# Performance work log

Measured on AMD Instinct MI355X. Metric: run time of the kernel, lower is better.

The kernel has to match this reference:

```python
import jax, jax.numpy as jnp
import numpy as np


def _deform_conv2d(x, offset, weight, stride=(1, 1), pad=(1, 1), dilation=(1, 1)):
    # x: [B,C,H,W]; offset: [B, 2*Goff*kh*kw, oh, ow]; weight: [OC, C//Gw, kh, kw]
    B, C, H, W = x.shape
    OC, Cg, kh, kw = weight.shape
    Gw = C // Cg
    K = kh * kw
    sh, sw = stride
    ph, pw = pad
    dh, dw = dilation
    oh = (H + 2 * ph - (dh * (kh - 1) + 1)) // sh + 1
    ow = (W + 2 * pw - (dw * (kw - 1) + 1)) // sw + 1
    Goff = offset.shape[1] // (2 * K)
    # torchvision layout: per offset group, per kernel tap k, (dy, dx)
    off = offset.reshape(B, Goff, K, 2, oh, ow)
    ki = jnp.arange(K) // kw  # kernel row per tap
    kj = jnp.arange(K) % kw   # kernel col per tap
    base_y = jnp.arange(oh) * sh - ph
    base_x = jnp.arange(ow) * sw - pw
    gy = (base_y[None, :] + (ki * dh)[:, None]).astype(x.dtype)  # [K, oh]
    gx = (base_x[None, :] + (kj * dw)[:, None]).astype(x.dtype)  # [K, ow]
    py = off[:, :, :, 0] + gy[None, None, :, :, None]  # [B,Goff,K,oh,ow]
    px = off[:, :, :, 1] + gx[None, None, :, None, :]
    cpg = C // Goff  # channels per offset group
    py = jnp.repeat(py, cpg, axis=1)  # [B,C,K,oh,ow]
    px = jnp.repeat(px, cpg, axis=1)
    xf = x.reshape(B, C, H * W)
    y0 = jnp.floor(py)
    x0 = jnp.floor(px)
    ty = py - y0
    tx = px - x0
    y0i = y0.astype(jnp.int32)
    x0i = x0.astype(jnp.int32)

    def gather(cy, cx):
        valid = (cy >= 0) & (cy < H) & (cx >= 0) & (cx < W)
        idx = jnp.clip(cy, 0, H - 1) * W + jnp.clip(cx, 0, W - 1)
        v = jnp.take_along_axis(xf, idx.reshape(B, C, -1), axis=2).reshape(idx.shape)
        return jnp.where(valid, v, jnp.zeros((), x.dtype))

    # bilinear sample, zero padding outside image (matches torchvision)
    v = (gather(y0i, x0i) * (1 - ty) * (1 - tx)
         + gather(y0i, x0i + 1) * (1 - ty) * tx
         + gather(y0i + 1, x0i) * ty * (1 - tx)
         + gather(y0i + 1, x0i + 1) * ty * tx)  # [B,C,K,oh,ow]
    v = v.reshape(B, Gw, Cg, K, oh, ow)
    wg = weight.reshape(Gw, OC // Gw, Cg, K)
    out = jnp.einsum('bgckhw,gock->bgohw', v, wg)
    return out.reshape(B, OC, oh, ow)


def setup_inputs() -> dict:
    key = jax.random.key(0)
    k1, k2, k3 = jax.random.split(key, 3)
    x = jax.random.normal(k1, (8, 64, 56, 56), dtype=jnp.float32)
    offset = jax.random.normal(k2, (8, 18, 56, 56), dtype=jnp.float32)
    weight = jax.random.normal(k3, (64, 64, 3, 3), dtype=jnp.float32) * 0.05
    return {"input": x, "offset": offset, "weight": weight}


def reference(input, offset, weight):
    return _deform_conv2d(input, offset, weight, stride=(1, 1), pad=(1, 1), dilation=(1, 1))
```

## Files before the change

### kernel.cpp

```cpp
#include <hip/hip_runtime.h>
#include <hip/hip_fp16.h>


typedef _Float16 f16x8 __attribute__((ext_vector_type(8)));
typedef float    f32x4 __attribute__((ext_vector_type(4)));

namespace {
constexpr int Bn = 8, Cn = 64, Hn = 56, Wn = 56;
constexpr int Kk = 9, OCn = 64;
constexpr int NPIX = 56 * 56;
constexpr int CK   = Cn * Kk;
constexpr int TP   = 32;
constexpr int TILES = NPIX / TP;
constexpr int XTILES = NPIX / 64;
constexpr int KSTEPS = CK / 32;
}

__device__ __forceinline__ __half2 u2h(unsigned u) {
    union { unsigned u; __half2 h; } x; x.u = u; return x.h;
}
__device__ __forceinline__ unsigned bcast_h(float f) {
    unsigned short hs = __half_as_ushort(__float2half(f));
    return (unsigned)hs * 0x10001u;
}
__device__ __forceinline__ void lds_barrier() {
    asm volatile("s_waitcnt lgkmcnt(0)" ::: "memory");
    __builtin_amdgcn_s_barrier();
}

__global__ __launch_bounds__(256) void prep_kernel(
    const float* __restrict__ x, const float* __restrict__ w,
    unsigned short* __restrict__ xh, unsigned short* __restrict__ wh2)
{
    const int tid = threadIdx.x;
    if (blockIdx.x >= 392) {
        const int i = (blockIdx.x - 392) * 256 + tid;
        if (i < OCn * CK) {
            const int j    = i & 7;
            const int lane = (i >> 3) & 63;
            const int rest = i >> 9;
            const int og   = rest / KSTEPS;
            const int oc   = og * 16 + (lane & 15);
            const int kglob = (rest % KSTEPS) * 32 + (lane >> 4) * 8 + j;
            const int tap = kglob >> 6;
            const int c   = kglob & 63;
            wh2[i] = __half_as_ushort(__float2half(w[oc * CK + c * Kk + tap]));
        }
        return;
    }
    __shared__ unsigned short lds[64][66];
    const int b  = blockIdx.x / XTILES;
    const int t0 = (blockIdx.x % XTILES) * 64;
    const float* xb = x + (size_t)b * Cn * NPIX;
    {
        const int hw0 = (tid & 15) * 4;
        #pragma unroll
        for (int i = 0; i < 4; ++i) {
            const int c = (tid >> 4) + i * 16;
            const float4 v = *(const float4*)(xb + (size_t)c * NPIX + t0 + hw0);
            lds[hw0 + 0][c] = __half_as_ushort(__float2half(v.x));
            lds[hw0 + 1][c] = __half_as_ushort(__float2half(v.y));
            lds[hw0 + 2][c] = __half_as_ushort(__float2half(v.z));
            lds[hw0 + 3][c] = __half_as_ushort(__float2half(v.w));
        }
    }
    __syncthreads();
    {
        const int co = (tid & 7) * 8;
        #pragma unroll
        for (int i = 0; i < 2; ++i) {
            const int hw = (tid >> 3) + i * 32;
            unsigned short tmp[8] __attribute__((aligned(16)));
            #pragma unroll
            for (int j = 0; j < 8; ++j) tmp[j] = lds[hw][co + j];
            *(uint4*)(xh + ((size_t)b * NPIX + t0 + hw) * Cn + co) = *(const uint4*)tmp;
        }
    }
}

__global__ __launch_bounds__(256, 4) void deform_fused(
    const unsigned short* __restrict__ xh, const float* __restrict__ off,
    const unsigned short* __restrict__ wh2, float* __restrict__ out)
{
    __shared__ uint4 smpw[Kk * TP];
    __shared__ int4  smpa[Kk * TP];
    __shared__ __align__(16) uint4 vbuf[3][8 * TP];

    const int tid = threadIdx.x;
    const int b  = blockIdx.x / TILES;
    const int p0 = (blockIdx.x % TILES) * TP;
    const unsigned short* xb = xh + (size_t)b * NPIX * Cn;
    const float* offb = off + (size_t)b * 18 * NPIX;

    for (int e = tid; e < Kk * TP; e += 256) {
        const int k  = e >> 5;
        const int px = e & 31;
        const int p  = p0 + px;
        const int oy = p / Wn, ox = p % Wn;
        const int ki = k / 3, kj = k % 3;
        const float offy = offb[(size_t)(2 * k)     * NPIX + p];
        const float offx = offb[(size_t)(2 * k + 1) * NPIX + p];
        const float py  = offy + (float)(oy - 1 + ki);
        const float pxv = offx + (float)(ox - 1 + kj);
        const float y0f = floorf(py), x0f = floorf(pxv);
        const float ty = py - y0f, tx = pxv - x0f;
        const int y0 = (int)y0f, x0 = (int)x0f;
        const int y1 = y0 + 1, x1 = x0 + 1;
        const bool vy0 = (y0 >= 0) & (y0 < Hn);
        const bool vy1 = (y1 >= 0) & (y1 < Hn);
        const bool vx0 = (x0 >= 0) & (x0 < Wn);
        const bool vx1 = (x1 >= 0) & (x1 < Wn);
        const int cy0 = min(max(y0, 0), Hn - 1);
        const int cy1 = min(max(y1, 0), Hn - 1);
        const int cx0 = min(max(x0, 0), Wn - 1);
        const int cx1 = min(max(x1, 0), Wn - 1);
        uint4 wq;
        wq.x = bcast_h((vy0 && vx0) ? (1.f - ty) * (1.f - tx) : 0.f);
        wq.y = bcast_h((vy0 && vx1) ? (1.f - ty) * tx         : 0.f);
        wq.z = bcast_h((vy1 && vx0) ? ty * (1.f - tx)         : 0.f);
        wq.w = bcast_h((vy1 && vx1) ? ty * tx                 : 0.f);
        int4 av;
        av.x = (cy0 * Wn + cx0) * Cn;
        av.y = (cy0 * Wn + cx1) * Cn;
        av.z = (cy1 * Wn + cx0) * Cn;
        av.w = (cy1 * Wn + cx1) * Cn;
        smpw[e] = wq;
        smpa[e] = av;
    }
    lds_barrier();

    const int oct = tid & 7;
    const int gpx = (tid >> 3) & 31;
    const int co  = oct * 8;

    const int lane = tid & 63;
    const int og   = tid >> 6;
    const int hi   = lane >> 4;
    const int lr   = lane & 15;
    const uint4* ab = (const uint4*)wh2 + (size_t)og * KSTEPS * 64 + lane;

    uint4 s0[3], s1[3], s2[3], s3[3], wqr[3];
    uint4 aF[2][2];
    f32x4 acc0 = {0.f, 0.f, 0.f, 0.f};
    f32x4 acc1 = {0.f, 0.f, 0.f, 0.f};

    auto stage = [&](int k) {
        const int sl = k % 3;
        const int m  = k * TP + gpx;
        const int4 av = smpa[m];
        wqr[sl] = smpw[m];
        s0[sl] = *(const uint4*)(xb + av.x + co);
        s1[sl] = *(const uint4*)(xb + av.y + co);
        s2[sl] = *(const uint4*)(xb + av.z + co);
        s3[sl] = *(const uint4*)(xb + av.w + co);
    };
    auto loadA = [&](int k) {
        const int sl = k & 1;
        aF[sl][0] = ab[(k * 2 + 0) * 64];
        aF[sl][1] = ab[(k * 2 + 1) * 64];
    };
    auto blend = [&](int k) {
        const int sl = k % 3;
        const __half2 w00 = u2h(wqr[sl].x), w01 = u2h(wqr[sl].y);
        const __half2 w10 = u2h(wqr[sl].z), w11 = u2h(wqr[sl].w);
        uint4 res;
        unsigned* rp = (unsigned*)&res;
        #pragma unroll
        for (int q = 0; q < 4; ++q) {
            __half2 a = __hmul2(w00, u2h(((const unsigned*)&s0[sl])[q]));
            a = __hfma2(w01, u2h(((const unsigned*)&s1[sl])[q]), a);
            a = __hfma2(w10, u2h(((const unsigned*)&s2[sl])[q]), a);
            a = __hfma2(w11, u2h(((const unsigned*)&s3[sl])[q]), a);
            rp[q] = *(const unsigned*)&a;
        }
        vbuf[sl][oct * TP + gpx] = res;
    };
    auto mfma = [&](int k) {
        const int sl = k % 3;
        #pragma unroll
        for (int kl = 0; kl < 2; ++kl) {
            const int octr = kl * 4 + hi;
            union { uint4 u; f16x8 h; } a, b0, b1;
            a.u  = aF[k & 1][kl];
            b0.u = vbuf[sl][octr * TP + lr];
            b1.u = vbuf[sl][octr * TP + 16 + lr];
            acc0 = __builtin_amdgcn_mfma_f32_16x16x32_f16(a.h, b0.h, acc0, 0, 0, 0);
            acc1 = __builtin_amdgcn_mfma_f32_16x16x32_f16(a.h, b1.h, acc1, 0, 0, 0);
        }
    };

    stage(0); stage(1); stage(2);
    loadA(0);
    blend(0);
    lds_barrier();

    #pragma unroll
    for (int k = 0; k < Kk; ++k) {
        if (k < Kk - 3) stage(k + 3);
        if (k < Kk - 1) loadA(k + 1);
        if (k < Kk - 1) blend(k + 1);
        mfma(k);
        lds_barrier();
    }

    float* ob = out + ((size_t)b * OCn + og * 16 + hi * 4) * NPIX + p0 + lr;
    #pragma unroll
    for (int r = 0; r < 4; ++r) {
        ob[(size_t)r * NPIX]      = acc0[r];
        ob[(size_t)r * NPIX + 16] = acc1[r];
    }
}

extern "C" void kernel_launch(void* const* d_in, const int* in_sizes, int n_in,
                              void* d_out, int out_size, void* d_ws, size_t ws_size,
                              hipStream_t stream) {
    const float* x   = (const float*)d_in[0];
    const float* off = (const float*)d_in[1];
    const float* w   = (const float*)d_in[2];
    float* out = (float*)d_out;
    unsigned short* wh2 = (unsigned short*)d_ws;
    unsigned short* xh  = (unsigned short*)((char*)d_ws + 131072);

    hipLaunchKernelGGL(prep_kernel, dim3(392 + 144), dim3(256), 0, stream, x, w, xh, wh2);
    hipLaunchKernelGGL(deform_fused, dim3(Bn * TILES), dim3(256), 0, stream,
                       xh, off, wh2, out);
}
```

Before: 21.67 us.

## Hand-schedule gather loads with inline asm and explicit vmcnt waits

The gather and weight-fragment loads become inline-asm global_load_dwordx4 instructions. Explicit s_waitcnt vmcnt counts and sched_barriers let each blend wait only on its own stage while later loads stay in flight, rather than relying on the compiler's conservative waits. The gather prefetch depth drops from three to two stages to save registers, and the launch-bounds occupancy hint goes from 4 to 3 blocks, giving the compiler more VGRPs. The risk is that the compiler treats the asm outputs as ready immediately, so correctness depends on the hand-counted waits. Fewer resident waves may also hide latency less well.

```diff
diff --git a/kernel.cpp b/kernel.cpp
--- a/kernel.cpp
+++ b/kernel.cpp
@@ -26,6 +26,9 @@
 __device__ __forceinline__ void lds_barrier() {
     asm volatile("s_waitcnt lgkmcnt(0)" ::: "memory");
     __builtin_amdgcn_s_barrier();
+}
+__device__ __forceinline__ void gld16(uint4& d, const unsigned short* p) {
+    asm volatile("global_load_dwordx4 %0, %1, off" : "=&v"(d) : "v"(p) : "memory");
 }
 
 __global__ __launch_bounds__(256) void prep_kernel(
@@ -78,7 +81,7 @@
     }
 }
 
-__global__ __launch_bounds__(256, 4) void deform_fused(
+__global__ __launch_bounds__(256, 3) void deform_fused(
     const unsigned short* __restrict__ xh, const float* __restrict__ off,
     const unsigned short* __restrict__ wh2, float* __restrict__ out)
 {
@@ -128,6 +131,7 @@
         smpa[e] = av;
     }
     lds_barrier();
+    asm volatile("s_waitcnt vmcnt(0)" ::: "memory");
 
     const int oct = tid & 7;
     const int gpx = (tid >> 3) & 31;
@@ -139,28 +143,28 @@
     const int lr   = lane & 15;
     const uint4* ab = (const uint4*)wh2 + (size_t)og * KSTEPS * 64 + lane;
 
-    uint4 s0[3], s1[3], s2[3], s3[3], wqr[3];
+    uint4 s0[2], s1[2], s2[2], s3[2], wqr[2];
     uint4 aF[2][2];
     f32x4 acc0 = {0.f, 0.f, 0.f, 0.f};
     f32x4 acc1 = {0.f, 0.f, 0.f, 0.f};
 
-    auto stage = [&](int k) {
-        const int sl = k % 3;
+    auto stageC = [&](int k) {
+        const int sl = k & 1;
         const int m  = k * TP + gpx;
         const int4 av = smpa[m];
         wqr[sl] = smpw[m];
-        s0[sl] = *(const uint4*)(xb + av.x + co);
-        s1[sl] = *(const uint4*)(xb + av.y + co);
-        s2[sl] = *(const uint4*)(xb + av.z + co);
-        s3[sl] = *(const uint4*)(xb + av.w + co);
+        gld16(s0[sl], xb + av.x + co);
+        gld16(s1[sl], xb + av.y + co);
+        gld16(s2[sl], xb + av.z + co);
+        gld16(s3[sl], xb + av.w + co);
     };
     auto loadA = [&](int k) {
         const int sl = k & 1;
-        aF[sl][0] = ab[(k * 2 + 0) * 64];
-        aF[sl][1] = ab[(k * 2 + 1) * 64];
+        gld16(aF[sl][0], (const unsigned short*)(ab + (k * 2 + 0) * 64));
+        gld16(aF[sl][1], (const unsigned short*)(ab + (k * 2 + 1) * 64));
     };
     auto blend = [&](int k) {
-        const int sl = k % 3;
+        const int sl = k & 1;
         const __half2 w00 = u2h(wqr[sl].x), w01 = u2h(wqr[sl].y);
         const __half2 w10 = u2h(wqr[sl].z), w11 = u2h(wqr[sl].w);
         uint4 res;
@@ -173,7 +177,7 @@
             a = __hfma2(w11, u2h(((const unsigned*)&s3[sl])[q]), a);
             rp[q] = *(const unsigned*)&a;
         }
-        vbuf[sl][oct * TP + gpx] = res;
+        vbuf[k % 3][oct * TP + gpx] = res;
     };
     auto mfma = [&](int k) {
         const int sl = k % 3;
@@ -189,15 +193,21 @@
         }
     };
 
-    stage(0); stage(1); stage(2);
+    stageC(0); stageC(1);
     loadA(0);
+    asm volatile("s_waitcnt vmcnt(6)" ::: "memory");
+    __builtin_amdgcn_sched_barrier(0);
     blend(0);
     lds_barrier();
 
     #pragma unroll
     for (int k = 0; k < Kk; ++k) {
-        if (k < Kk - 3) stage(k + 3);
+        if (k < Kk - 2) stageC(k + 2);
         if (k < Kk - 1) loadA(k + 1);
+        if (k < Kk - 2)      asm volatile("s_waitcnt vmcnt(6)" ::: "memory");
+        else if (k == Kk - 2) asm volatile("s_waitcnt vmcnt(2)" ::: "memory");
+        else                  asm volatile("s_waitcnt vmcnt(0)" ::: "memory");
+        __builtin_amdgcn_sched_barrier(0);
         if (k < Kk - 1) blend(k + 1);
         mfma(k);
         lds_barrier();
```

New measurement: 22.00 us. Within noise of the previous version (+1.5%).
